# Performance work log

Measured on AMD Instinct MI355X. Metric: run time of the kernel, lower is better.

Reference implementation:

```python
import jax, jax.numpy as jnp
import numpy as np

B = 32768      # batch
N_IN = 128     # input nodes
L = 8          # topological layers
W = 256        # nodes per layer
K = 16         # fan-in per node


def setup_inputs() -> dict:
    key = jax.random.key(0)
    k_x, k_w, k_b, k_e = jax.random.split(key, 4)
    inputs = jax.random.normal(k_x, (B, N_IN), dtype=jnp.float32)
    # scale weights down so sigmoid isn't saturated with fan-in 16
    weights = jax.random.normal(k_w, (L, W, K), dtype=jnp.float32) * 0.25
    biases = jax.random.normal(k_b, (L, W), dtype=jnp.float32) * 0.1
    # DAG-valid edges: layer l may only gather from the N_IN + l*W already-computed nodes
    ek = jax.random.split(k_e, L)
    edge_idx = jnp.stack([
        jax.random.randint(ek[l], (W, K), 0, N_IN + l * W, dtype=jnp.int32)
        for l in range(L)
    ])  # [L, W, K]
    return {"inputs": inputs, "weights": weights, "biases": biases,
            "edge_idx": edge_idx}


def reference(inputs, weights, biases, edge_idx):
    # values buffer starts as the input-node activations: [B, N_IN]
    vals = inputs
    n_layers = weights.shape[0]
    for l in range(n_layers):
        gathered = vals[:, edge_idx[l]]                      # [B, W, K] per-node gather
        pre = jnp.einsum('bwk,wk->bw', gathered, weights[l]) + biases[l]
        vals = jnp.concatenate([vals, jax.nn.sigmoid(pre)], axis=1)
    # output nodes are the last layer, concatenated in order
    return vals[:, -W:]
```

## Files before the change

### kernel.cpp

```cpp
#include <hip/hip_runtime.h>
#include <hip/hip_bf16.h>
#include <hip/hip_fp16.h>


#define NB   32768
#define NIN  128
#define NL   8
#define NW   256
#define NK   16
#define RPB  16
#define STORED (NIN + (NL - 1) * NW)
#define NPARAM (NL * NW * NK)

typedef __fp16 fp16v2 __attribute__((ext_vector_type(2)));

__device__ __forceinline__ unsigned pk16(float a, float b) {
    fp16v2 p = __builtin_amdgcn_cvt_pkrtz(a, b);
    return __builtin_bit_cast(unsigned, p);
}

__device__ __forceinline__ __half2 as_h2(unsigned u) {
    return __builtin_bit_cast(__half2, u);
}

__device__ __forceinline__ float fast_sigmoid(float x) {
    return __builtin_amdgcn_rcpf(1.0f + __expf(-x));
}

__device__ __forceinline__ void fma_feat(__half2 acc[4], __half2 w2, uint4 p) {
    acc[0] = __hfma2(as_h2(p.x), w2, acc[0]);
    acc[1] = __hfma2(as_h2(p.y), w2, acc[1]);
    acc[2] = __hfma2(as_h2(p.z), w2, acc[2]);
    acc[3] = __hfma2(as_h2(p.w), w2, acc[3]);
}

template <bool PRE>
__global__ __launch_bounds__(256, 2)
void ffn_gather_kernel(const float* __restrict__ inputs,
                       const float* __restrict__ weights,
                       const float* __restrict__ biases,
                       const int*   __restrict__ edge_idx,
                       const int*   __restrict__ idxb,
                       const unsigned* __restrict__ wpk,
                       float* __restrict__ out)
{
    __shared__ uint4 valsA[STORED];
    __shared__ uint4 valsB[STORED];

    const int t = threadIdx.x;
    const long long row0 = (long long)blockIdx.x * RPB;
    const char* vbaseA = (const char*)valsA;
    const char* vbaseB = (const char*)valsB;

    {
        const int f = t & 127;
        const long long r0 = row0 + ((t >> 7) << 3);
        float v[8];
        #pragma unroll
        for (int r = 0; r < 8; ++r) v[r] = inputs[(r0 + r) * NIN + f];
        uint4 p;
        p.x = pk16(v[0], v[1]);
        p.y = pk16(v[2], v[3]);
        p.z = pk16(v[4], v[5]);
        p.w = pk16(v[6], v[7]);
        if (t < NIN) valsA[f] = p; else valsB[f] = p;
    }
    __syncthreads();

    #pragma unroll
    for (int l = 0; l < NL; ++l) {
        const int base = (l * NW + t) * NK;

        const float b = biases[l * NW + t];
        __half2 accA[4], accB[4];
        const __half2 bb = __float2half2_rn(b);
        #pragma unroll
        for (int j = 0; j < 4; ++j) { accA[j] = bb; accB[j] = bb; }

        #pragma unroll
        for (int kk = 0; kk < NK / 4; ++kk) {
            int4 o4;
            __half2 w0, w1, w2, w3;
            if (PRE) {
                o4 = ((const int4*)(idxb + base))[kk];
                uint4 wp = ((const uint4*)(wpk + base))[kk];
                w0 = as_h2(wp.x); w1 = as_h2(wp.y);
                w2 = as_h2(wp.z); w3 = as_h2(wp.w);
            } else {
                int4 i4 = ((const int4*)(edge_idx + base))[kk];
                o4.x = i4.x << 4; o4.y = i4.y << 4;
                o4.z = i4.z << 4; o4.w = i4.w << 4;
                float4 w4 = ((const float4*)(weights + base))[kk];
                w0 = __float2half2_rn(w4.x);
                w1 = __float2half2_rn(w4.y);
                w2 = __float2half2_rn(w4.z);
                w3 = __float2half2_rn(w4.w);
            }
            const uint4 a0 = *(const uint4*)(vbaseA + o4.x);
            const uint4 b0 = *(const uint4*)(vbaseB + o4.x);
            const uint4 a1 = *(const uint4*)(vbaseA + o4.y);
            const uint4 b1 = *(const uint4*)(vbaseB + o4.y);
            const uint4 a2 = *(const uint4*)(vbaseA + o4.z);
            const uint4 b2 = *(const uint4*)(vbaseB + o4.z);
            const uint4 a3 = *(const uint4*)(vbaseA + o4.w);
            const uint4 b3 = *(const uint4*)(vbaseB + o4.w);
            fma_feat(accA, w0, a0);
            fma_feat(accB, w0, b0);
            fma_feat(accA, w1, a1);
            fma_feat(accB, w1, b1);
            fma_feat(accA, w2, a2);
            fma_feat(accB, w2, b2);
            fma_feat(accA, w3, a3);
            fma_feat(accB, w3, b3);
        }

        float sA[8], sB[8];
        #pragma unroll
        for (int j = 0; j < 4; ++j) {
            sA[2 * j + 0] = fast_sigmoid(__low2float(accA[j]));
            sA[2 * j + 1] = fast_sigmoid(__high2float(accA[j]));
            sB[2 * j + 0] = fast_sigmoid(__low2float(accB[j]));
            sB[2 * j + 1] = fast_sigmoid(__high2float(accB[j]));
        }

        if (l < NL - 1) {
            uint4 pA, pB;
            pA.x = pk16(sA[0], sA[1]); pA.y = pk16(sA[2], sA[3]);
            pA.z = pk16(sA[4], sA[5]); pA.w = pk16(sA[6], sA[7]);
            pB.x = pk16(sB[0], sB[1]); pB.y = pk16(sB[2], sB[3]);
            pB.z = pk16(sB[4], sB[5]); pB.w = pk16(sB[6], sB[7]);
            valsA[NIN + l * NW + t] = pA;
            valsB[NIN + l * NW + t] = pB;
            __syncthreads();
        } else {
            #pragma unroll
            for (int r = 0; r < 8; ++r) {
                out[(row0 + r) * NW + t]     = sA[r];
                out[(row0 + 8 + r) * NW + t] = sB[r];
            }
        }
    }
}

__global__ __launch_bounds__(256)
void balance_prepass_kernel(const float* __restrict__ weights,
                            const int* __restrict__ edge_idx,
                            int* __restrict__ idxb,
                            unsigned* __restrict__ wpk)
{
    const int t = blockIdx.x * 256 + threadIdx.x;
    const int lane = threadIdx.x & 63;
    const int base = t * NK;

    int   idxv[NK];
    float wv[NK];
    #pragma unroll
    for (int j = 0; j < NK; ++j) {
        idxv[j] = edge_idx[base + j];
        wv[j]   = weights[base + j];
    }

    unsigned long long cntp = 0;
    #pragma unroll
    for (int j = 0; j < NK; ++j)
        cntp += 1ull << ((idxv[j] & 7) * 8);

    unsigned long long x = cntp;
    x += x << 8;
    x += x << 16;
    x += x << 32;
    unsigned long long cur = x << 8;

    const int rot = (2 * (lane & 7) + ((lane >> 3) & 7)) & 15;
    #pragma unroll
    for (int j = 0; j < NK; ++j) {
        const int g   = idxv[j] & 7;
        const int pos = (int)((cur >> (g * 8)) & 0xFF);
        cur += 1ull << (g * 8);
        const int slot = (pos + rot) & 15;
        idxb[base + slot] = idxv[j] << 4;
        wpk [base + slot] = pk16(wv[j], wv[j]);
    }
}

extern "C" void kernel_launch(void* const* d_in, const int* in_sizes, int n_in,
                              void* d_out, int out_size, void* d_ws, size_t ws_size,
                              hipStream_t stream)
{
    const float* inputs   = (const float*)d_in[0];
    const float* weights  = (const float*)d_in[1];
    const float* biases   = (const float*)d_in[2];
    const int*   edge_idx = (const int*)d_in[3];
    float* out = (float*)d_out;

    dim3 grid(NB / RPB);
    dim3 block(NW);

    const size_t need = (size_t)NPARAM * 4 * 2;
    if (ws_size >= need) {
        int*      idxb = (int*)d_ws;
        unsigned* wpk  = (unsigned*)((char*)d_ws + (size_t)NPARAM * 4);
        balance_prepass_kernel<<<NL * NW / 256, 256, 0, stream>>>(
            weights, edge_idx, idxb, wpk);
        ffn_gather_kernel<true><<<grid, block, 0, stream>>>(
            inputs, weights, biases, edge_idx, idxb, wpk, out);
    } else {
        ffn_gather_kernel<false><<<grid, block, 0, stream>>>(
            inputs, weights, biases, edge_idx, nullptr, nullptr, out);
    }
}
```

Before: 134.1 us.

## Replicate early features at shifted LDS offset to rebalance gather bank conflicts

Adds a second LDS copy of the first 639 feature rows (inputs plus early layers) at a base offset that lands in a different bank group. The prepass now runs one block per layer and chooses, per node group, which edges read from the shifted copy so that each bank group sees an even load. The aim is fewer LDS bank conflicts in the random gather. In exchange it adds extra LDS stores for layers 0-1 and per-load offset selects, and it grows LDS use to 80KB per block, which may cut how many blocks fit on a CU.

```diff
diff --git a/kernel.cpp b/kernel.cpp
--- a/kernel.cpp
+++ b/kernel.cpp
@@ -11,8 +11,15 @@
 #define RPB  16
 #define STORED (NIN + (NL - 1) * NW)
 #define NPARAM (NL * NW * NK)
+#define NREP   639
+#define A1BASE 61456
+#define B1BASE 71696
+#define D0OFF  30720
+#define D1OFF  10240
+#define LDSBYTES 81920
 
 typedef __fp16 fp16v2 __attribute__((ext_vector_type(2)));
+typedef unsigned long long u64;
 
 __device__ __forceinline__ unsigned pk16(float a, float b) {
     fp16v2 p = __builtin_amdgcn_cvt_pkrtz(a, b);
@@ -44,13 +51,10 @@
                        const unsigned* __restrict__ wpk,
                        float* __restrict__ out)
 {
-    __shared__ uint4 valsA[STORED];
-    __shared__ uint4 valsB[STORED];
+    __shared__ __align__(16) char vals[LDSBYTES];
 
     const int t = threadIdx.x;
     const long long row0 = (long long)blockIdx.x * RPB;
-    const char* vbaseA = (const char*)valsA;
-    const char* vbaseB = (const char*)valsB;
 
     {
         const int f = t & 127;
@@ -63,7 +67,13 @@
         p.y = pk16(v[2], v[3]);
         p.z = pk16(v[4], v[5]);
         p.w = pk16(v[6], v[7]);
-        if (t < NIN) valsA[f] = p; else valsB[f] = p;
+        if (t < NIN) {
+            *(uint4*)(vals + f * 16)           = p;
+            *(uint4*)(vals + A1BASE + f * 16)  = p;
+        } else {
+            *(uint4*)(vals + D0OFF + f * 16)   = p;
+            *(uint4*)(vals + B1BASE + f * 16)  = p;
+        }
     }
     __syncthreads();
 
@@ -96,14 +106,20 @@
                 w2 = __float2half2_rn(w4.z);
                 w3 = __float2half2_rn(w4.w);
             }
-            const uint4 a0 = *(const uint4*)(vbaseA + o4.x);
-            const uint4 b0 = *(const uint4*)(vbaseB + o4.x);
-            const uint4 a1 = *(const uint4*)(vbaseA + o4.y);
-            const uint4 b1 = *(const uint4*)(vbaseB + o4.y);
-            const uint4 a2 = *(const uint4*)(vbaseA + o4.z);
-            const uint4 b2 = *(const uint4*)(vbaseB + o4.z);
-            const uint4 a3 = *(const uint4*)(vbaseA + o4.w);
-            const uint4 b3 = *(const uint4*)(vbaseB + o4.w);
+            int4 b4;
+            b4.x = o4.x + (o4.x >= A1BASE ? D1OFF : D0OFF);
+            b4.y = o4.y + (o4.y >= A1BASE ? D1OFF : D0OFF);
+            b4.z = o4.z + (o4.z >= A1BASE ? D1OFF : D0OFF);
+            b4.w = o4.w + (o4.w >= A1BASE ? D1OFF : D0OFF);
+
+            const uint4 a0 = *(const uint4*)(vals + o4.x);
+            const uint4 b0 = *(const uint4*)(vals + b4.x);
+            const uint4 a1 = *(const uint4*)(vals + o4.y);
+            const uint4 b1 = *(const uint4*)(vals + b4.y);
+            const uint4 a2 = *(const uint4*)(vals + o4.z);
+            const uint4 b2 = *(const uint4*)(vals + b4.z);
+            const uint4 a3 = *(const uint4*)(vals + o4.w);
+            const uint4 b3 = *(const uint4*)(vals + b4.w);
             fma_feat(accA, w0, a0);
             fma_feat(accB, w0, b0);
             fma_feat(accA, w1, a1);
@@ -129,8 +145,15 @@
             pA.z = pk16(sA[4], sA[5]); pA.w = pk16(sA[6], sA[7]);
             pB.x = pk16(sB[0], sB[1]); pB.y = pk16(sB[2], sB[3]);
             pB.z = pk16(sB[4], sB[5]); pB.w = pk16(sB[6], sB[7]);
-            valsA[NIN + l * NW + t] = pA;
-            valsB[NIN + l * NW + t] = pB;
+            const int F = NIN + l * NW + t;
+            *(uint4*)(vals + F * 16)          = pA;
+            *(uint4*)(vals + D0OFF + F * 16)  = pB;
+            if (l < 2) {
+                if (F < NREP) {
+                    *(uint4*)(vals + A1BASE + F * 16) = pA;
+                    *(uint4*)(vals + B1BASE + F * 16) = pB;
+                }
+            }
             __syncthreads();
         } else {
             #pragma unroll
@@ -143,42 +166,114 @@
 }
 
 __global__ __launch_bounds__(256)
-void balance_prepass_kernel(const float* __restrict__ weights,
-                            const int* __restrict__ edge_idx,
-                            int* __restrict__ idxb,
-                            unsigned* __restrict__ wpk)
+void emit_kernel(const float* __restrict__ weights,
+                 const int* __restrict__ edge_idx,
+                 int* __restrict__ idxb,
+                 unsigned* __restrict__ wpk)
 {
-    const int t = blockIdx.x * 256 + threadIdx.x;
-    const int lane = threadIdx.x & 63;
-    const int base = t * NK;
+    __shared__ u64 s_cnt[NW];
+    __shared__ u64 s_ch[NW];
+    __shared__ u64 s_take[NW];
+
+    const int l = blockIdx.x;
+    const int t = threadIdx.x;
+    const int base = (l * NW + t) * NK;
+    const int lane = t & 63;
 
     int   idxv[NK];
     float wv[NK];
+    u64 cnt = 0, ch = 0;
     #pragma unroll
     for (int j = 0; j < NK; ++j) {
         idxv[j] = edge_idx[base + j];
         wv[j]   = weights[base + j];
-    }
-
-    unsigned long long cntp = 0;
+        const int g = idxv[j] & 7;
+        cnt += 1ull << (g * 8);
+        if (idxv[j] < NREP) ch += 1ull << (g * 8);
+    }
+    s_cnt[t] = cnt;
+    s_ch[t]  = ch;
+    __syncthreads();
+
+    if ((t & 7) == 0) {
+        u64 chu[8], tku[8];
+        u64 D = 0, CH = 0;
+        #pragma unroll
+        for (int r = 0; r < 8; ++r) {
+            chu[r] = s_ch[t + r];
+            D  += s_cnt[t + r];
+            CH += chu[r];
+            tku[r] = 0;
+        }
+        int pg[8], CHg[8];
+        int pfx = 0, minp = 0, chi = 0x7fffffff;
+        #pragma unroll
+        for (int g = 0; g < 8; ++g) {
+            pfx += (int)((D >> (g * 8)) & 0xFF) - 16;
+            pg[g] = pfx;
+            if (pfx < minp) minp = pfx;
+            CHg[g] = (int)((CH >> (g * 8)) & 0xFF);
+            const int hi = CHg[g] - pfx;
+            if (hi < chi) chi = hi;
+        }
+        int c = -minp; if (c < 0) c = 0;
+        if (c > chi) c = (chi < 0) ? 0 : chi;
+        #pragma unroll
+        for (int g = 0; g < 8; ++g) {
+            int s = c + pg[g];
+            s = s < 0 ? 0 : s;
+            if (s > CHg[g]) s = CHg[g];
+            int rem = s;
+            #pragma unroll
+            for (int r = 0; r < 8; ++r) {
+                const int av = (int)((chu[r] >> (g * 8)) & 0xFF);
+                const int tk = rem < av ? rem : av;
+                rem -= tk;
+                tku[r] += (u64)tk << (g * 8);
+            }
+        }
+        #pragma unroll
+        for (int r = 0; r < 8; ++r) s_take[t + r] = tku[r];
+    }
+    __syncthreads();
+    const u64 take = s_take[t];
+
+    u64 usedc = 0;
+    int fg[NK], sh[NK];
+    #pragma unroll
+    for (int j = 0; j < NK; ++j) {
+        const int g = idxv[j] & 7;
+        int s_ = 0;
+        if (idxv[j] < NREP) {
+            const int uc = (int)((usedc >> (g * 8)) & 0xFF);
+            const int tk = (int)((take  >> (g * 8)) & 0xFF);
+            s_ = (uc < tk) ? 1 : 0;
+            usedc += 1ull << (g * 8);
+        }
+        sh[j] = s_;
+        fg[j] = (g + s_) & 7;
+    }
+
+    u64 fcnt = 0;
     #pragma unroll
     for (int j = 0; j < NK; ++j)
-        cntp += 1ull << ((idxv[j] & 7) * 8);
-
-    unsigned long long x = cntp;
+        fcnt += 1ull << (fg[j] * 8);
+
+    u64 x = fcnt;
     x += x << 8;
     x += x << 16;
     x += x << 32;
-    unsigned long long cur = x << 8;
+    u64 cur = x << 8;
 
     const int rot = (2 * (lane & 7) + ((lane >> 3) & 7)) & 15;
     #pragma unroll
     for (int j = 0; j < NK; ++j) {
-        const int g   = idxv[j] & 7;
+        const int g   = fg[j];
         const int pos = (int)((cur >> (g * 8)) & 0xFF);
         cur += 1ull << (g * 8);
         const int slot = (pos + rot) & 15;
-        idxb[base + slot] = idxv[j] << 4;
+        idxb[base + slot] = sh[j] ? (A1BASE + (idxv[j] << 4))
+                                  : (idxv[j] << 4);
         wpk [base + slot] = pk16(wv[j], wv[j]);
     }
 }
@@ -200,8 +295,7 @@
     if (ws_size >= need) {
         int*      idxb = (int*)d_ws;
         unsigned* wpk  = (unsigned*)((char*)d_ws + (size_t)NPARAM * 4);
-        balance_prepass_kernel<<<NL * NW / 256, 256, 0, stream>>>(
-            weights, edge_idx, idxb, wpk);
+        emit_kernel<<<NL, NW, 0, stream>>>(weights, edge_idx, idxb, wpk);
         ffn_gather_kernel<true><<<grid, block, 0, stream>>>(
             inputs, weights, biases, edge_idx, idxb, wpk, out);
     } else {
```

Result: slower. 146.7 us (+9.4%).
